# Performance work log

Measured on AMD Instinct MI355X. Metric: run time of the kernel, lower is better.

The kernel has to match this reference:

```python
import math
import jax, jax.numpy as jnp
import numpy as np

B, S, HID, H = 2, 1024, 2048, 16
D = HID // H
HEAVY_RATIO = 0.1
RECENT_RATIO = 0.1
ROPE_BASE = 10000.0
N_KEEP_DIMS = 6  # eviction zeroes all but the 6 largest-|k| dims


def setup_inputs() -> dict:
    key = jax.random.key(0)
    k1, k2, k3, k4, k5 = jax.random.split(key, 5)
    std = 0.02
    hidden_states = jax.random.normal(k1, (B, S, HID), jnp.float32)
    wq = jax.random.normal(k2, (HID, HID), jnp.float32) * std
    wk = jax.random.normal(k3, (HID, HID), jnp.float32) * std
    wv = jax.random.normal(k4, (HID, HID), jnp.float32) * std
    wo = jax.random.normal(k5, (HID, HID), jnp.float32) * std
    neg = jnp.finfo(jnp.float32).min
    causal = jnp.tril(jnp.ones((S, S), bool))
    attention_mask = jnp.broadcast_to(
        jnp.where(causal, 0.0, neg)[None, None], (B, 1, S, S)
    ).astype(jnp.float32)
    return {"hidden_states": hidden_states, "wq": wq, "wk": wk, "wv": wv,
            "wo": wo, "attention_mask": attention_mask}


def _rotate_half(x):
    return jnp.concatenate([-x[..., D // 2:], x[..., :D // 2]], axis=-1)


def _apply_rope(q, k):
    inv_freq = 1.0 / (ROPE_BASE ** (jnp.arange(0, D, 2, dtype=jnp.float32) / D))
    t = jnp.arange(S, dtype=jnp.float32)
    freqs = jnp.outer(t, inv_freq)              # [S, D/2]
    emb = jnp.concatenate([freqs, freqs], -1)   # [S, D]
    cos = jnp.cos(emb)[None, None]              # [1,1,S,D]
    sin = jnp.sin(emb)[None, None]
    return q * cos + _rotate_half(q) * sin, k * cos + _rotate_half(k) * sin


def _h2o_attention(q, k, heavy_budget, recent_budget):
    """Faithful vectorized form of low_dimension_attention.

    The torch loop mutates key_states in place by zeroing the (D-6)
    smallest-magnitude dims of one evicted token per step. Since the
    small-dim set is fixed per (b,h) and zeroing is idempotent, we carry a
    boolean evicted mask instead of the mutated key tensor.
    """
    cache_budget = heavy_budget + recent_budget
    scale = 1.0 / math.sqrt(D)
    # small_dimensions: computed once at first trigger (t = cache_budget+1)
    # from the first cache_budget (unmutated) keys.
    mean_abs = jnp.abs(k[:, :, :cache_budget, :]).mean(axis=2)      # [B,H,D]
    ranks = jnp.argsort(jnp.argsort(mean_abs, axis=-1), axis=-1)
    small_mask = ranks < (D - N_KEEP_DIMS)                          # [B,H,D]
    sidx = jnp.arange(S)

    def step(carry, xs):
        hist, evicted, prev_attn = carry
        t, q_t = xs                                                 # q_t: [B,H,D]
        pred = t > cache_budget
        limit = t - recent_budget if recent_budget > 0 else t
        # eviction score = inf-mask history + previous step's raw scores
        scores = jnp.where(sidx < limit, hist + prev_attn, jnp.inf)  # [B,H,S]
        idx = jnp.argmin(scores, axis=-1)                            # [B,H]
        do = pred & (sidx[None, None, :] == idx[..., None])          # [B,H,S]
        evicted = evicted | do
        hist = jnp.where(do, jnp.inf, hist)
        k_eff = jnp.where(evicted[..., None] & small_mask[:, :, None, :], 0.0, k)
        attn = jnp.einsum('bhd,bhsd->bhs', q_t, k_eff) * scale
        attn = jnp.where(sidx <= t, attn, 0.0)
        return (hist, evicted, attn), attn

    init = (jnp.zeros((B, H, S), jnp.float32),
            jnp.zeros((B, H, S), bool),
            jnp.zeros((B, H, S), jnp.float32))
    q_seq = jnp.moveaxis(q, 2, 0)                                    # [S,B,H,D]
    _, rows = jax.lax.scan(step, init, (jnp.arange(S), q_seq))       # [S,B,H,S]
    return jnp.moveaxis(rows, 0, 2)                                  # [B,H,S,S]


def reference(hidden_states, wq, wk, wv, wo, attention_mask):
    heavy_budget = int(HEAVY_RATIO * S)
    recent_budget = int(RECENT_RATIO * S)
    q = (hidden_states @ wq).reshape(B, S, H, D).transpose(0, 2, 1, 3)
    k = (hidden_states @ wk).reshape(B, S, H, D).transpose(0, 2, 1, 3)
    v = (hidden_states @ wv).reshape(B, S, H, D).transpose(0, 2, 1, 3)
    q, k = _apply_rope(q, k)
    attn_weights = _h2o_attention(q, k, heavy_budget, recent_budget)  # [B,H,S,S]
    attn_weights = jnp.maximum(attn_weights + attention_mask,
                               jnp.finfo(jnp.float32).min)
    attn_weights = jax.nn.softmax(attn_weights, axis=-1)
    out = jnp.einsum('bhqk,bhkd->bhqd', attn_weights, v)
    out = out.transpose(0, 2, 1, 3).reshape(B, S, HID)
    return out @ wo
```

## Files before the change

### kernel.cpp

```cpp
#include <hip/hip_runtime.h>
#include <math.h>

#define S_LEN    1024
#define NHEAD    16
#define DHEAD    128
#define HIDDEN   2048
#define BATCH    2
#define BH       32
#define CACHE_B  204
#define RECENT_B 102
#define QK_SCALE 0.08838834764831845f

typedef float v2f __attribute__((ext_vector_type(2)));
typedef float f32x4 __attribute__((ext_vector_type(4)));
typedef short short8v __attribute__((ext_vector_type(8)));

__device__ __forceinline__ unsigned short f2bf(float f) {
  unsigned u = __float_as_uint(f);
  u += 0x7fffu + ((u >> 16) & 1u);
  return (unsigned short)(u >> 16);
}
__device__ __forceinline__ float bf2f(unsigned short h) {
  return __uint_as_float(((unsigned)h) << 16);
}

__device__ __forceinline__ void gl16(const void* g, void* l) {
  __builtin_amdgcn_global_load_lds(
      (const __attribute__((address_space(1))) unsigned int*)g,
      (__attribute__((address_space(3))) unsigned int*)l, 16, 0, 0);
}

__device__ __forceinline__ void mfma_b(f32x4& d, short8v a, short8v b) {
  asm("v_mfma_f32_16x16x32_bf16 %0, %1, %2, %0" : "+v"(d) : "v"(a), "v"(b));
}

__global__ __launch_bounds__(256) void split_a(
    const float* __restrict__ X, unsigned short* __restrict__ hi,
    unsigned short* __restrict__ lo) {
  const size_t i = ((size_t)blockIdx.x * 256 + threadIdx.x) * 4;
  const float4 v = *(const float4*)&X[i];
  const float f[4] = {v.x, v.y, v.z, v.w};
  unsigned short h[4], l[4];
#pragma unroll
  for (int j = 0; j < 4; ++j) {
    h[j] = f2bf(f[j]);
    l[j] = f2bf(f[j] - bf2f(h[j]));
  }
  *(ushort4*)&hi[i] = make_ushort4(h[0], h[1], h[2], h[3]);
  *(ushort4*)&lo[i] = make_ushort4(l[0], l[1], l[2], l[3]);
}

__global__ __launch_bounds__(256) void split_T(
    const float* __restrict__ W0, const float* __restrict__ W1,
    const float* __restrict__ W2, unsigned short* __restrict__ outB) {
  __shared__ float Ts[64][65];
  const float* W = (blockIdx.z == 0) ? W0 : ((blockIdx.z == 1) ? W1 : W2);
  unsigned short* hiT = outB + (size_t)blockIdx.z * 8388608u;
  unsigned short* loT = hiT + 4194304u;
  const int k0 = blockIdx.y * 64, n0 = blockIdx.x * 64;
  const int r = threadIdx.x >> 4, c4 = (threadIdx.x & 15) * 4;
#pragma unroll
  for (int it = 0; it < 4; ++it) {
    const float4 v =
        *(const float4*)&W[(size_t)(k0 + it * 16 + r) * HIDDEN + n0 + c4];
    Ts[it * 16 + r][c4 + 0] = v.x;
    Ts[it * 16 + r][c4 + 1] = v.y;
    Ts[it * 16 + r][c4 + 2] = v.z;
    Ts[it * 16 + r][c4 + 3] = v.w;
  }
  __syncthreads();
#pragma unroll
  for (int it = 0; it < 4; ++it) {
    const int n = it * 16 + r;
    unsigned short h[4], l[4];
#pragma unroll
    for (int j = 0; j < 4; ++j) {
      const float f = Ts[c4 + j][n];
      h[j] = f2bf(f);
      l[j] = f2bf(f - bf2f(h[j]));
    }
    const size_t o = (size_t)(n0 + n) * HIDDEN + k0 + c4;
    *(ushort4*)&hiT[o] = make_ushort4(h[0], h[1], h[2], h[3]);
    *(ushort4*)&loT[o] = make_ushort4(l[0], l[1], l[2], l[3]);
  }
}

template <int MODE>
__global__ __launch_bounds__(256) void gemm_mfma(
    const unsigned short* __restrict__ Ahi,
    const unsigned short* __restrict__ Alo,
    const unsigned short* __restrict__ WT, float* __restrict__ C0) {
  __shared__ unsigned short AhS[128][32];
  __shared__ unsigned short AlS[128][32];
  __shared__ unsigned short BhS[128][32];
  __shared__ unsigned short BlS[128][32];
  const int tid = threadIdx.x;
  const int lane = tid & 63;
  const int wv = tid >> 6;
  const int wr = wv >> 1, wc = wv & 1;
  const int m0 = blockIdx.y * 128, n0 = blockIdx.x * 128;
  const unsigned short* BhiT =
      WT + (MODE == 0 ? (size_t)blockIdx.z * 8388608u : (size_t)0);
  const unsigned short* BloT = BhiT + 4194304u;

  f32x4 acc[4][4];
#pragma unroll
  for (int i = 0; i < 4; ++i)
#pragma unroll
    for (int j = 0; j < 4; ++j) acc[i][j] = (f32x4)(0.0f);

  const int r_st = tid >> 2;
  const int kc_st = (tid & 3) * 8;

  for (int k0 = 0; k0 < HIDDEN; k0 += 32) {
#pragma unroll
    for (int l = 0; l < 2; ++l) {
      const int r = r_st + l * 64;
      const size_t ga = (size_t)(m0 + r) * HIDDEN + (k0 + kc_st);
      const size_t gb = (size_t)(n0 + r) * HIDDEN + (k0 + kc_st);
      gl16(Ahi + ga, &AhS[r][kc_st]);
      gl16(Alo + ga, &AlS[r][kc_st]);
      gl16(BhiT + gb, &BhS[r][kc_st]);
      gl16(BloT + gb, &BlS[r][kc_st]);
    }
    __syncthreads();
    const int mrow = lane & 15;
    const int kb = (lane >> 4) * 8;
    short8v ah[4], al[4], bh[4], bl[4];
#pragma unroll
    for (int i = 0; i < 4; ++i) {
      ah[i] = *(const short8v*)&AhS[wr * 64 + i * 16 + mrow][kb];
      al[i] = *(const short8v*)&AlS[wr * 64 + i * 16 + mrow][kb];
      bh[i] = *(const short8v*)&BhS[wc * 64 + i * 16 + mrow][kb];
      bl[i] = *(const short8v*)&BlS[wc * 64 + i * 16 + mrow][kb];
    }
#pragma unroll
    for (int i = 0; i < 4; ++i)
#pragma unroll
      for (int j = 0; j < 4; ++j) {
        mfma_b(acc[i][j], ah[i], bh[j]);
        mfma_b(acc[i][j], al[i], bh[j]);
        mfma_b(acc[i][j], ah[i], bl[j]);
      }
    __syncthreads();
  }

  float* C = C0;
  if (MODE == 0) C += (size_t)blockIdx.z * ((size_t)BH * S_LEN * DHEAD);
#pragma unroll
  for (int i = 0; i < 4; ++i) {
    const int mbase = m0 + wr * 64 + i * 16 + ((lane >> 4) * 4);
#pragma unroll
    for (int j = 0; j < 4; ++j) {
      const int n = n0 + wc * 64 + j * 16 + (lane & 15);
#pragma unroll
      for (int rg = 0; rg < 4; ++rg) {
        const int m = mbase + rg;
        const float val = acc[i][j][rg];
        if (MODE == 0) {
          const int b = m >> 10, s = m & (S_LEN - 1);
          const int h = n >> 7, d = n & (DHEAD - 1);
          C[(((size_t)(b * NHEAD + h) * S_LEN + s) * DHEAD) + d] = val;
        } else {
          C[(size_t)m * HIDDEN + n] = val;
        }
      }
    }
  }
}

__global__ __launch_bounds__(256) void rope_qk(float* __restrict__ Q,
                                               float* __restrict__ K) {
  int g = blockIdx.x * 4 + (threadIdx.x >> 6);
  int lane = threadIdx.x & 63;
  int s = g & (S_LEN - 1);
  double invf = exp(-((double)(2 * lane) / 128.0) * log(10000.0));
  float angle = (float)s * (float)invf;
  float c = (float)cos((double)angle);
  float sn = (float)sin((double)angle);
  size_t base = (size_t)g * DHEAD;
  float q0 = Q[base + lane], q1 = Q[base + lane + 64];
  Q[base + lane] = q0 * c - q1 * sn;
  Q[base + lane + 64] = q1 * c + q0 * sn;
  float k0 = K[base + lane], k1 = K[base + lane + 64];
  K[base + lane] = k0 * c - k1 * sn;
  K[base + lane + 64] = k1 * c + k0 * sn;
}

__global__ __launch_bounds__(128) void keep_pack(
    const float* __restrict__ Q, const float* __restrict__ K,
    float* __restrict__ Qp, float* __restrict__ KpT) {
  int bh = blockIdx.x;
  int d = threadIdx.x;
  __shared__ float ma[128];
  __shared__ int kf[128];
  __shared__ int kidx[8];
  const float* Kb = K + (size_t)bh * S_LEN * DHEAD;
  const float* Qb = Q + (size_t)bh * S_LEN * DHEAD;
  float sum = 0.0f;
  for (int s = 0; s < CACHE_B; ++s) sum += fabsf(Kb[(size_t)s * DHEAD + d]);
  ma[d] = sum / 204.0f;
  __syncthreads();
  float v = ma[d];
  int rank = 0;
  for (int e = 0; e < 128; ++e) {
    float u = ma[e];
    rank += (u < v) || (u == v && e < d);
  }
  int keep = (rank >= 128 - 6);
  kf[d] = keep;
  __syncthreads();
  if (keep) {
    int pos = 0;
    for (int e = 0; e < d; ++e) pos += kf[e];
    kidx[pos] = d;
  }
  __syncthreads();
  int i0 = kidx[0], i1 = kidx[1], i2 = kidx[2];
  int i3 = kidx[3], i4 = kidx[4], i5 = kidx[5];
  float* Kt = KpT + (size_t)bh * 6 * S_LEN;
  for (int s = threadIdx.x; s < S_LEN; s += 128) {
    size_t src = (size_t)s * DHEAD;
    size_t dst = ((size_t)bh * S_LEN + s) * 8;
    Qp[dst + 0] = Qb[src + i0]; Qp[dst + 1] = Qb[src + i1];
    Qp[dst + 2] = Qb[src + i2]; Qp[dst + 3] = Qb[src + i3];
    Qp[dst + 4] = Qb[src + i4]; Qp[dst + 5] = Qb[src + i5];
    Kt[0 * S_LEN + s] = Kb[src + i0];
    Kt[1 * S_LEN + s] = Kb[src + i1];
    Kt[2 * S_LEN + s] = Kb[src + i2];
    Kt[3 * S_LEN + s] = Kb[src + i3];
    Kt[4 * S_LEN + s] = Kb[src + i4];
    Kt[5 * S_LEN + s] = Kb[src + i5];
  }
}

__global__ __launch_bounds__(256) void qkt_scores(
    const float* __restrict__ Q, const float* __restrict__ K,
    float* __restrict__ Af) {
  if (blockIdx.x > blockIdx.y) return;
  __shared__ float Qs[16][132];
  __shared__ float Ks[16][132];
  const int bh = blockIdx.z;
  const int tid = threadIdx.x;
  const int tx = tid & 15, ty = tid >> 4;
  const int m0 = blockIdx.y * 128, n0 = blockIdx.x * 128;
  const float* Qb = Q + (size_t)bh * S_LEN * DHEAD;
  const float* Kb = K + (size_t)bh * S_LEN * DHEAD;
  v2f acc[8][4];
#pragma unroll
  for (int i = 0; i < 8; ++i)
#pragma unroll
    for (int p = 0; p < 4; ++p) acc[i][p] = (v2f)(0.0f);

  for (int k0 = 0; k0 < DHEAD; k0 += 16) {
#pragma unroll
    for (int l = 0; l < 2; ++l) {
      int f = tid + l * 256;
      int r = f >> 2, c = (f & 3) * 4;
      const float4 q = *(const float4*)&Qb[(size_t)(m0 + r) * DHEAD + k0 + c];
      Qs[c + 0][r] = q.x; Qs[c + 1][r] = q.y;
      Qs[c + 2][r] = q.z; Qs[c + 3][r] = q.w;
      const float4 kv = *(const float4*)&Kb[(size_t)(n0 + r) * DHEAD + k0 + c];
      Ks[c + 0][r] = kv.x; Ks[c + 1][r] = kv.y;
      Ks[c + 2][r] = kv.z; Ks[c + 3][r] = kv.w;
    }
    __syncthreads();
#pragma unroll
    for (int kk = 0; kk < 16; ++kk) {
      float av[8];
      v2f bv[4];
      *(float4*)&av[0] = *(float4*)&Qs[kk][ty * 4];
      *(float4*)&av[4] = *(float4*)&Qs[kk][64 + ty * 4];
      const float4 b0 = *(const float4*)&Ks[kk][tx * 4];
      const float4 b1 = *(const float4*)&Ks[kk][64 + tx * 4];
      bv[0] = (v2f){b0.x, b0.y};
      bv[1] = (v2f){b0.z, b0.w};
      bv[2] = (v2f){b1.x, b1.y};
      bv[3] = (v2f){b1.z, b1.w};
#pragma unroll
      for (int i = 0; i < 8; ++i) {
        const v2f a2 = (v2f){av[i], av[i]};
#pragma unroll
        for (int p = 0; p < 4; ++p) acc[i][p] = a2 * bv[p] + acc[i][p];
      }
    }
    __syncthreads();
  }
  float* Cb = Af + (size_t)bh * S_LEN * S_LEN;
#pragma unroll
  for (int gi = 0; gi < 2; ++gi)
#pragma unroll
    for (int i = 0; i < 4; ++i) {
      const int t = m0 + gi * 64 + ty * 4 + i;
      const int ia = gi * 4 + i;
#pragma unroll
      for (int gj = 0; gj < 2; ++gj) {
        const int s = n0 + gj * 64 + tx * 4;
        float4 o;
        o.x = acc[ia][gj * 2 + 0].x * QK_SCALE;
        o.y = acc[ia][gj * 2 + 0].y * QK_SCALE;
        o.z = acc[ia][gj * 2 + 1].x * QK_SCALE;
        o.w = acc[ia][gj * 2 + 1].y * QK_SCALE;
        *(float4*)&Cb[(size_t)t * S_LEN + s] = o;
      }
    }
}

template <int CTRL, int RMASK>
__device__ __forceinline__ float dpp_fmin(float x) {
  const int xi = __builtin_bit_cast(int, x);
  const int y = __builtin_amdgcn_update_dpp(xi, xi, CTRL, RMASK, 0xF, false);
  return fminf(x, __builtin_bit_cast(float, y));
}
__device__ __forceinline__ float wave_min_f32(float x) {
  x = dpp_fmin<0x111, 0xF>(x);
  x = dpp_fmin<0x112, 0xF>(x);
  x = dpp_fmin<0x114, 0xF>(x);
  x = dpp_fmin<0x118, 0xF>(x);
  x = dpp_fmin<0x142, 0xA>(x);
  x = dpp_fmin<0x143, 0xC>(x);
  return __builtin_bit_cast(
      float, __builtin_amdgcn_readlane(__builtin_bit_cast(int, x), 63));
}

__global__ __launch_bounds__(64, 1) void scan_evict(
    const float* __restrict__ Af, int* __restrict__ evt) {
  __shared__ int evt_lds[S_LEN];
  const int bh = blockIdx.x;
  const int lane = threadIdx.x;
  const float* Ab = Af + (size_t)bh * S_LEN * S_LEN;
  int* evtb = evt + bh * S_LEN;

  {
    const int4 big = make_int4(0x7fffffff, 0x7fffffff, 0x7fffffff, 0x7fffffff);
#pragma unroll
    for (int j = 0; j < 4; ++j) *(int4*)&evt_lds[j * 256 + lane * 4] = big;
  }

  unsigned evmask = 0;
  unsigned elig = (lane < 6) ? 0xFFFFu : (lane == 6 ? 0x7Fu : 0u);

  const float* lb = Ab + lane * 16;
  float4 A0[4], A1[4], A2[4], A3[4], A4[4], A5[4];

#define SB() __builtin_amdgcn_sched_barrier(0)

#define LDROW(R, r)                                      \
  do {                                                   \
    int r_ = (r);                                        \
    r_ = r_ > 1022 ? 1022 : r_;                          \
    const float* rb = lb + (size_t)r_ * S_LEN;           \
    R[0] = *(const float4*)(rb + 0);                     \
    R[1] = *(const float4*)(rb + 4);                     \
    R[2] = *(const float4*)(rb + 8);                     \
    R[3] = *(const float4*)(rb + 12);                    \
  } while (0)

#define STEP(R, T)                                                          \
  do {                                                                      \
    const int t_ = (T);                                                     \
    const int snew = t_ - 103;      \
    elig |= ((snew >> 4) == lane) ? (1u << (snew & 15)) : 0u;               \
    const unsigned ue = elig & ~evmask;                                     \
    float fv[16];                                                           \
    _Pragma("unroll") for (int p = 0; p < 4; ++p) {                         \
      fv[p * 4 + 0] = ((ue >> (p * 4 + 0)) & 1u) ? R[p].x : INFINITY;       \
      fv[p * 4 + 1] = ((ue >> (p * 4 + 1)) & 1u) ? R[p].y : INFINITY;       \
      fv[p * 4 + 2] = ((ue >> (p * 4 + 2)) & 1u) ? R[p].z : INFINITY;       \
      fv[p * 4 + 3] = ((ue >> (p * 4 + 3)) & 1u) ? R[p].w : INFINITY;       \
    }                                                                       \
            \
    float m8[8]; int s8[8];                                                 \
    _Pragma("unroll") for (int i = 0; i < 8; ++i) {                         \
      m8[i] = fminf(fv[2 * i], fv[2 * i + 1]);                              \
      s8[i] = (fv[2 * i] <= fv[2 * i + 1]) ? (2 * i) : (2 * i + 1);         \
    }                                                                       \
    float m4[4]; int s4[4];                                                 \
    _Pragma("unroll") for (int i = 0; i < 4; ++i) {                         \
      m4[i] = fminf(m8[2 * i], m8[2 * i + 1]);                              \
      s4[i] = (m8[2 * i] <= m8[2 * i + 1]) ? s8[2 * i] : s8[2 * i + 1];     \
    }                                                                       \
    float m2[2]; int s2[2];                                                 \
    m2[0] = fminf(m4[0], m4[1]); s2[0] = (m4[0] <= m4[1]) ? s4[0] : s4[1];  \
    m2[1] = fminf(m4[2], m4[3]); s2[1] = (m4[2] <= m4[3]) ? s4[2] : s4[3];  \
    const float vmin = fminf(m2[0], m2[1]);                                 \
    const int bloc = (m2[0] <= m2[1]) ? s2[0] : s2[1];                      \
    const float best = wave_min_f32(vmin);                                  \
    const unsigned long long msk = __ballot(vmin == best);                  \
    const int winner = __ffsll(msk) - 1;        \
    if (lane == winner) {                                                   \
      evmask |= 1u << bloc;                                                 \
      evt_lds[lane * 16 + bloc] = t_;     \
    }                                                                       \
  } while (0)

  LDROW(A0, 204); LDROW(A1, 205); LDROW(A2, 206);
  LDROW(A3, 207); LDROW(A4, 208); LDROW(A5, 209);
  SB();

  for (int g = 0; g < 136; ++g) {
    const int t0 = 205 + g * 6;
    STEP(A0, t0 + 0); LDROW(A0, t0 + 5); SB();
    STEP(A1, t0 + 1); LDROW(A1, t0 + 6); SB();
    STEP(A2, t0 + 2); LDROW(A2, t0 + 7); SB();
    STEP(A3, t0 + 3); LDROW(A3, t0 + 8); SB();
    STEP(A4, t0 + 4); LDROW(A4, t0 + 9); SB();
    STEP(A5, t0 + 5); LDROW(A5, t0 + 10); SB();
  }
  STEP(A0, 1021);
  STEP(A1, 1022);
  STEP(A2, 1023);

  asm volatile("s_waitcnt lgkmcnt(0)" ::: "memory");
  SB();
#pragma unroll
  for (int j = 0; j < 4; ++j)
    *(int4*)&evtb[j * 256 + lane * 4] =
        *(const int4*)&evt_lds[j * 256 + lane * 4];
#undef LDROW
#undef STEP
#undef SB
}

__global__ __launch_bounds__(256) void attn_av(
    const float* __restrict__ Af, const float* __restrict__ Qp,
    const float* __restrict__ KpT, const int* __restrict__ evt,
    const float* __restrict__ V, float* __restrict__ AO) {
  const int t0 = blockIdx.x * 8;
  const int bh = blockIdx.y;
  __shared__ float P[8][S_LEN];
  __shared__ float rinv[8];
  const int tid = threadIdx.x;
  const int lane = tid & 63, wave = tid >> 6;
  const float* Ab = Af + (size_t)bh * S_LEN * S_LEN;
  const int* eb = evt + bh * S_LEN;
  const float* Kt = KpT + (size_t)bh * 6 * S_LEN;

  for (int rr = 0; rr < 2; ++rr) {
    const int r = wave * 2 + rr;
    const int t = t0 + r;
    float qp[6];
#pragma unroll
    for (int j = 0; j < 6; ++j) qp[j] = Qp[((size_t)bh * S_LEN + t) * 8 + j];
    float vals[16];
    float m = -INFINITY;
#pragma unroll
    for (int i = 0; i < 16; ++i) {
      const int s = lane + i * 64;
      const float full = Ab[(size_t)t * S_LEN + s];
      float low = qp[0] * Kt[s];
      low += qp[1] * Kt[S_LEN + s];
      low += qp[2] * Kt[2 * S_LEN + s];
      low += qp[3] * Kt[3 * S_LEN + s];
      low += qp[4] * Kt[4 * S_LEN + s];
      low += qp[5] * Kt[5 * S_LEN + s];
      const int ev = eb[s];
      const float sc = (ev <= t) ? (QK_SCALE * low) : full;
      vals[i] = sc;
      m = fmaxf(m, (s <= t) ? sc : -INFINITY);
    }
    for (int off = 32; off; off >>= 1) m = fmaxf(m, __shfl_xor(m, off, 64));
    float sum = 0.0f;
#pragma unroll
    for (int i = 0; i < 16; ++i) {
      const int s = lane + i * 64;
      const float e = expf(vals[i] - m);
      const float p = (s <= t) ? e : 0.0f;
      sum += p;
      P[r][s] = p;
    }
    for (int off = 32; off; off >>= 1) sum += __shfl_xor(sum, off, 64);
    if (lane == 0) rinv[r] = 1.0f / sum;
  }
  __syncthreads();

  const int NC = (t0 + 8) >> 2;
  const float* Vb = V + (size_t)bh * S_LEN * DHEAD;
  const int d2 = lane * 2;
  float accx[8], accy[8];
#pragma unroll
  for (int r = 0; r < 8; ++r) { accx[r] = 0.0f; accy[r] = 0.0f; }
  for (int c = wave; c < NC; c += 4) {
    const int s0 = c * 4;
    float4 p4[8];
#pragma unroll
    for (int r = 0; r < 8; ++r) p4[r] = *(const float4*)&P[r][s0];
    const float2 v0 = *(const float2*)&Vb[(size_t)(s0 + 0) * DHEAD + d2];
    const float2 v1 = *(const float2*)&Vb[(size_t)(s0 + 1) * DHEAD + d2];
    const float2 v2 = *(const float2*)&Vb[(size_t)(s0 + 2) * DHEAD + d2];
    const float2 v3 = *(const float2*)&Vb[(size_t)(s0 + 3) * DHEAD + d2];
#pragma unroll
    for (int r = 0; r < 8; ++r) {
      accx[r] += p4[r].x * v0.x + p4[r].y * v1.x + p4[r].z * v2.x +
                 p4[r].w * v3.x;
      accy[r] += p4[r].x * v0.y + p4[r].y * v1.y + p4[r].z * v2.y +
                 p4[r].w * v3.y;
    }
  }
  __syncthreads();
  float* red = &P[0][0];
#pragma unroll
  for (int r = 0; r < 8; ++r) {
    float2 pr; pr.x = accx[r]; pr.y = accy[r];
    *(float2*)&red[((wave * 8 + r) << 7) + d2] = pr;
  }
  __syncthreads();
  const int r = tid >> 5;
  const int d4 = (tid & 31) * 4;
  const int t = t0 + r;
  float4 o = make_float4(0.f, 0.f, 0.f, 0.f);
#pragma unroll
  for (int w = 0; w < 4; ++w) {
    const float4 part = *(const float4*)&red[((w * 8 + r) << 7) + d4];
    o.x += part.x; o.y += part.y; o.z += part.z; o.w += part.w;
  }
  const float ri = rinv[r];
  o.x *= ri; o.y *= ri; o.z *= ri; o.w *= ri;
  const int b = bh >> 4, h = bh & 15;
  *(float4*)&AO[((size_t)(b * S_LEN + t)) * HIDDEN + h * DHEAD + d4] = o;
}

extern "C" void kernel_launch(void* const* d_in, const int* in_sizes, int n_in,
                              void* d_out, int out_size, void* d_ws,
                              size_t ws_size, hipStream_t stream) {
  const float* hs = (const float*)d_in[0];
  const float* wq = (const float*)d_in[1];
  const float* wk = (const float*)d_in[2];
  const float* wv = (const float*)d_in[3];
  const float* wo = (const float*)d_in[4];
  float* out = (float*)d_out;

  const size_t SZ_QKV = (size_t)BH * S_LEN * DHEAD;
  float* Q = (float*)d_ws;
  float* K = Q + SZ_QKV;
  float* V = K + SZ_QKV;
  float* Af = V + SZ_QKV;
  float* Qp = Af + (size_t)BH * S_LEN * S_LEN;
  float* KpT = Qp + (size_t)BH * S_LEN * 8;
  int* evt = (int*)(KpT + (size_t)BH * S_LEN * 8);
  float* AO = (float*)(evt + BH * S_LEN);

  unsigned short* U = (unsigned short*)Af;
  unsigned short* wT = U;
  unsigned short* hs_hi = U + 25165824u;
  unsigned short* hs_lo = hs_hi + 4194304u;
  unsigned short* ao_hi = U;
  unsigned short* ao_lo = U + 4194304u;
  unsigned short* woT = U + 8388608u;

  split_T<<<dim3(32, 32, 3), 256, 0, stream>>>(wq, wk, wv, wT);
  split_a<<<dim3(4096), 256, 0, stream>>>(hs, hs_hi, hs_lo);
  gemm_mfma<0><<<dim3(16, 16, 3), 256, 0, stream>>>(hs_hi, hs_lo, wT, Q);
  rope_qk<<<dim3(BH * S_LEN / 4), 256, 0, stream>>>(Q, K);
  keep_pack<<<dim3(BH), 128, 0, stream>>>(Q, K, Qp, KpT);
  qkt_scores<<<dim3(8, 8, BH), 256, 0, stream>>>(Q, K, Af);
  scan_evict<<<dim3(BH), 64, 0, stream>>>(Af, evt);
  attn_av<<<dim3(S_LEN / 8, BH), 256, 0, stream>>>(Af, Qp, KpT, evt, V, AO);
  split_a<<<dim3(4096), 256, 0, stream>>>(AO, ao_hi, ao_lo);
  split_T<<<dim3(32, 32, 1), 256, 0, stream>>>(wo, wo, wo, woT);
  gemm_mfma<1><<<dim3(16, 16, 1), 256, 0, stream>>>(ao_hi, ao_lo, woT, out);
}
```

Before: 1.002 ms.

## Warp-specialize eviction scan with producer waves staging rows into double-buffered LDS

Result: slower. 1.027 ms (+2.6%).

```diff
diff --git a/kernel.cpp b/kernel.cpp
--- a/kernel.cpp
+++ b/kernel.cpp
@@ -323,103 +323,100 @@
       float, __builtin_amdgcn_readlane(__builtin_bit_cast(int, x), 63));
 }
 
-__global__ __launch_bounds__(64, 1) void scan_evict(
+__global__ __launch_bounds__(576, 1) void scan_evict(
     const float* __restrict__ Af, int* __restrict__ evt) {
-  __shared__ int evt_lds[S_LEN];
+  __shared__ float buf[2][8][S_LEN];
   const int bh = blockIdx.x;
-  const int lane = threadIdx.x;
+  const int tid = threadIdx.x;
+  const int lane = tid & 63;
+  const int wv = tid >> 6;
   const float* Ab = Af + (size_t)bh * S_LEN * S_LEN;
   int* evtb = evt + bh * S_LEN;
 
-  {
+  if (wv < 8) {
+    const float* rb = Ab + (size_t)(204 + wv) * S_LEN;
+#pragma unroll
+    for (int c = 0; c < 4; ++c) {
+      const int w = c * 64 + lane;
+      const int g = w ^ ((w >> 3) & 7);
+      gl16(rb + g * 4, &buf[0][wv][c * 256 + lane * 4]);
+    }
+  } else {
     const int4 big = make_int4(0x7fffffff, 0x7fffffff, 0x7fffffff, 0x7fffffff);
-#pragma unroll
-    for (int j = 0; j < 4; ++j) *(int4*)&evt_lds[j * 256 + lane * 4] = big;
-  }
+    int4* e4 = (int4*)evtb;
+#pragma unroll
+    for (int j = 0; j < 4; ++j) e4[j * 64 + lane] = big;
+  }
+  __syncthreads();
 
   unsigned evmask = 0;
   unsigned elig = (lane < 6) ? 0xFFFFu : (lane == 6 ? 0x7Fu : 0u);
 
-  const float* lb = Ab + lane * 16;
-  float4 A0[4], A1[4], A2[4], A3[4], A4[4], A5[4];
-
-#define SB() __builtin_amdgcn_sched_barrier(0)
-
-#define LDROW(R, r)                                      \
-  do {                                                   \
-    int r_ = (r);                                        \
-    r_ = r_ > 1022 ? 1022 : r_;                          \
-    const float* rb = lb + (size_t)r_ * S_LEN;           \
-    R[0] = *(const float4*)(rb + 0);                     \
-    R[1] = *(const float4*)(rb + 4);                     \
-    R[2] = *(const float4*)(rb + 8);                     \
-    R[3] = *(const float4*)(rb + 12);                    \
-  } while (0)
-
-#define STEP(R, T)                                                          \
-  do {                                                                      \
-    const int t_ = (T);                                                     \
-    const int snew = t_ - 103;      \
-    elig |= ((snew >> 4) == lane) ? (1u << (snew & 15)) : 0u;               \
-    const unsigned ue = elig & ~evmask;                                     \
-    float fv[16];                                                           \
-    _Pragma("unroll") for (int p = 0; p < 4; ++p) {                         \
-      fv[p * 4 + 0] = ((ue >> (p * 4 + 0)) & 1u) ? R[p].x : INFINITY;       \
-      fv[p * 4 + 1] = ((ue >> (p * 4 + 1)) & 1u) ? R[p].y : INFINITY;       \
-      fv[p * 4 + 2] = ((ue >> (p * 4 + 2)) & 1u) ? R[p].z : INFINITY;       \
-      fv[p * 4 + 3] = ((ue >> (p * 4 + 3)) & 1u) ? R[p].w : INFINITY;       \
-    }                                                                       \
-            \
-    float m8[8]; int s8[8];                                                 \
-    _Pragma("unroll") for (int i = 0; i < 8; ++i) {                         \
-      m8[i] = fminf(fv[2 * i], fv[2 * i + 1]);                              \
-      s8[i] = (fv[2 * i] <= fv[2 * i + 1]) ? (2 * i) : (2 * i + 1);         \
-    }                                                                       \
-    float m4[4]; int s4[4];                                                 \
-    _Pragma("unroll") for (int i = 0; i < 4; ++i) {                         \
-      m4[i] = fminf(m8[2 * i], m8[2 * i + 1]);                              \
-      s4[i] = (m8[2 * i] <= m8[2 * i + 1]) ? s8[2 * i] : s8[2 * i + 1];     \
-    }                                                                       \
-    float m2[2]; int s2[2];                                                 \
-    m2[0] = fminf(m4[0], m4[1]); s2[0] = (m4[0] <= m4[1]) ? s4[0] : s4[1];  \
-    m2[1] = fminf(m4[2], m4[3]); s2[1] = (m4[2] <= m4[3]) ? s4[2] : s4[3];  \
-    const float vmin = fminf(m2[0], m2[1]);                                 \
-    const int bloc = (m2[0] <= m2[1]) ? s2[0] : s2[1];                      \
-    const float best = wave_min_f32(vmin);                                  \
-    const unsigned long long msk = __ballot(vmin == best);                  \
-    const int winner = __ffsll(msk) - 1;        \
-    if (lane == winner) {                                                   \
-      evmask |= 1u << bloc;                                                 \
-      evt_lds[lane * 16 + bloc] = t_;     \
-    }                                                                       \
-  } while (0)
-
-  LDROW(A0, 204); LDROW(A1, 205); LDROW(A2, 206);
-  LDROW(A3, 207); LDROW(A4, 208); LDROW(A5, 209);
-  SB();
-
-  for (int g = 0; g < 136; ++g) {
-    const int t0 = 205 + g * 6;
-    STEP(A0, t0 + 0); LDROW(A0, t0 + 5); SB();
-    STEP(A1, t0 + 1); LDROW(A1, t0 + 6); SB();
-    STEP(A2, t0 + 2); LDROW(A2, t0 + 7); SB();
-    STEP(A3, t0 + 3); LDROW(A3, t0 + 8); SB();
-    STEP(A4, t0 + 4); LDROW(A4, t0 + 9); SB();
-    STEP(A5, t0 + 5); LDROW(A5, t0 + 10); SB();
-  }
-  STEP(A0, 1021);
-  STEP(A1, 1022);
-  STEP(A2, 1023);
-
-  asm volatile("s_waitcnt lgkmcnt(0)" ::: "memory");
-  SB();
-#pragma unroll
-  for (int j = 0; j < 4; ++j)
-    *(int4*)&evtb[j * 256 + lane * 4] =
-        *(const int4*)&evt_lds[j * 256 + lane * 4];
-#undef LDROW
-#undef STEP
-#undef SB
+  for (int blk = 0; blk < 103; ++blk) {
+    if (wv < 8) {
+      if (blk + 1 < 103) {
+        int row = 204 + (blk + 1) * 8 + wv;
+        row = row > 1022 ? 1022 : row;
+        const float* rb = Ab + (size_t)row * S_LEN;
+        float* dst = &buf[(blk + 1) & 1][wv][0];
+#pragma unroll
+        for (int c = 0; c < 4; ++c) {
+          const int w = c * 64 + lane;
+          const int g = w ^ ((w >> 3) & 7);
+          gl16(rb + g * 4, dst + c * 256 + lane * 4);
+        }
+      }
+    } else {
+      const float* bc = &buf[blk & 1][0][0];
+      const int t0 = 205 + blk * 8;
+#pragma unroll
+      for (int u = 0; u < 8; ++u) {
+        const int t = t0 + u;
+        if (t > 1023) break;
+        f32x4 cur[4];
+#pragma unroll
+        for (int p = 0; p < 4; ++p) {
+          const int pc = lane * 4 + p;
+          const int ph = pc ^ ((pc >> 3) & 7);
+          cur[p] = *(const f32x4*)&bc[(size_t)u * S_LEN + ph * 4];
+        }
+        const int snew = t - 103;
+        elig |= ((snew >> 4) == lane) ? (1u << (snew & 15)) : 0u;
+        const unsigned ue = elig & ~evmask;
+        float fv[16];
+#pragma unroll
+        for (int b = 0; b < 16; ++b)
+          fv[b] = ((ue >> b) & 1u) ? cur[b >> 2][b & 3] : INFINITY;
+        float m8[8]; int s8[8];
+#pragma unroll
+        for (int i = 0; i < 8; ++i) {
+          m8[i] = fminf(fv[2 * i], fv[2 * i + 1]);
+          s8[i] = (fv[2 * i] <= fv[2 * i + 1]) ? (2 * i) : (2 * i + 1);
+        }
+        float m4[4]; int s4[4];
+#pragma unroll
+        for (int i = 0; i < 4; ++i) {
+          m4[i] = fminf(m8[2 * i], m8[2 * i + 1]);
+          s4[i] = (m8[2 * i] <= m8[2 * i + 1]) ? s8[2 * i] : s8[2 * i + 1];
+        }
+        float m2[2]; int s2[2];
+        m2[0] = fminf(m4[0], m4[1]);
+        s2[0] = (m4[0] <= m4[1]) ? s4[0] : s4[1];
+        m2[1] = fminf(m4[2], m4[3]);
+        s2[1] = (m4[2] <= m4[3]) ? s4[2] : s4[3];
+        const float vmin = fminf(m2[0], m2[1]);
+        const int bloc = (m2[0] <= m2[1]) ? s2[0] : s2[1];
+        const float best = wave_min_f32(vmin);
+        const unsigned long long msk = __ballot(vmin == best);
+        const int winner = __ffsll(msk) - 1;
+        if (lane == winner) {
+          evmask |= 1u << bloc;
+          evtb[lane * 16 + bloc] = t;
+        }
+      }
+    }
+    __syncthreads();
+  }
 }
 
 __global__ __launch_bounds__(256) void attn_av(
@@ -554,7 +551,7 @@
   rope_qk<<<dim3(BH * S_LEN / 4), 256, 0, stream>>>(Q, K);
   keep_pack<<<dim3(BH), 128, 0, stream>>>(Q, K, Qp, KpT);
   qkt_scores<<<dim3(8, 8, BH), 256, 0, stream>>>(Q, K, Af);
-  scan_evict<<<dim3(BH), 64, 0, stream>>>(Af, evt);
+  scan_evict<<<dim3(BH), 576, 0, stream>>>(Af, evt);
   attn_av<<<dim3(S_LEN / 8, BH), 256, 0, stream>>>(Af, Qp, KpT, evt, V, AO);
   split_a<<<dim3(4096), 256, 0, stream>>>(AO, ao_hi, ao_lo);
   split_T<<<dim3(32, 32, 1), 256, 0, stream>>>(wo, wo, wo, woT);
```
